# Performance work log

Measured on AMD Instinct MI355X. Metric: run time of the kernel, lower is better.

Reference implementation:

```python
import jax, jax.numpy as jnp
import numpy as np

DIM = 256
HEADS = 8
DIM_HEAD = 64
INNER = HEADS * DIM_HEAD  # 512
SCALE = DIM_HEAD ** -0.5
EPS = 1e-5


def _layernorm(x, w, b):
    mu = jnp.mean(x, axis=-1, keepdims=True)
    var = jnp.var(x, axis=-1, keepdims=True)
    return (x - mu) * jax.lax.rsqrt(var + EPS) * w + b


def setup_inputs() -> dict:
    key = jax.random.key(0)
    ks = jax.random.split(key, 20)
    B, N, M, H, W = 8, 4096, 256, 64, 64
    s = 0.02
    inp = {
        "feat": jax.random.normal(ks[0], (B, N, DIM), jnp.float32),
        "center": jax.random.normal(ks[1], (B, M, DIM), jnp.float32),
        "pos": jax.random.normal(ks[2], (B, DIM, H, W), jnp.float32),
        "center_pos": jax.random.normal(ks[3], (B, M, DIM), jnp.float32),
        # projection weights stored [in, out] so y = x @ W
        "Wq": jax.random.normal(ks[4], (DIM, INNER), jnp.float32) * s,
        "Wk": jax.random.normal(ks[5], (DIM, INNER), jnp.float32) * s,
        "Wv1": jax.random.normal(ks[6], (DIM, INNER), jnp.float32) * s,
        "Wv2": jax.random.normal(ks[7], (DIM, INNER), jnp.float32) * s,
        "Wo1": jax.random.normal(ks[8], (INNER, DIM), jnp.float32) * s,
        "Wo2": jax.random.normal(ks[9], (INNER, DIM), jnp.float32) * s,
        "ln1_w": jnp.ones((DIM,), jnp.float32),
        "ln1_b": jnp.zeros((DIM,), jnp.float32),
        "ln2_w": jnp.ones((DIM,), jnp.float32),
        "ln2_b": jnp.zeros((DIM,), jnp.float32),
        "ffn1_W1": jax.random.normal(ks[10], (DIM, DIM), jnp.float32) * s,
        "ffn1_W2": jax.random.normal(ks[11], (DIM, DIM), jnp.float32) * s,
        "ffn1_b2": jnp.zeros((DIM,), jnp.float32),
        "ffn2_W1": jax.random.normal(ks[12], (DIM, DIM), jnp.float32) * s,
        "ffn2_W2": jax.random.normal(ks[13], (DIM, DIM), jnp.float32) * s,
        "ffn2_b2": jnp.zeros((DIM,), jnp.float32),
    }
    return inp


def reference(feat, center, pos, center_pos, Wq, Wk, Wv1, Wv2, Wo1, Wo2,
              ln1_w, ln1_b, ln2_w, ln2_b, ffn1_W1, ffn1_W2, ffn1_b2,
              ffn2_W1, ffn2_W2, ffn2_b2):
    B = feat.shape[0]
    # pos: [B, C, H, W] -> [B, N, C]
    pos_f = pos.reshape(B, DIM, -1).transpose(0, 2, 1)
    q = (feat + pos_f) @ Wq            # [B, N, INNER]
    k = (center + center_pos) @ Wk     # [B, M, INNER]
    v1 = feat @ Wv1                    # [B, N, INNER]
    v2 = center @ Wv2                  # [B, M, INNER]

    def split(x):  # [B, T, h*d] -> [B, h, T, d]
        return x.reshape(B, x.shape[1], HEADS, DIM_HEAD).transpose(0, 2, 1, 3)

    q, k, v1, v2 = split(q), split(k), split(v1), split(v2)
    attn = jnp.einsum("bhnd,bhmd->bhnm", q, k) * SCALE  # [B, h, N, M]
    attn1 = jax.nn.softmax(attn, axis=-2)  # over N (queries)
    attn2 = jax.nn.softmax(attn, axis=-1)  # over M (keys)
    out_feat = jnp.einsum("bhnm,bhmd->bhnd", attn2, v2)    # [B, h, N, d]
    out_center = jnp.einsum("bhnm,bhnd->bhmd", attn1, v1)  # [B, h, M, d]

    def merge(x):  # [B, h, T, d] -> [B, T, h*d]
        return x.transpose(0, 2, 1, 3).reshape(B, x.shape[2], INNER)

    out_feat = merge(out_feat) @ Wo1 + feat
    out_center = merge(out_center) @ Wo2 + center
    out_feat = _layernorm(out_feat, ln1_w, ln1_b)
    out_center = _layernorm(out_center, ln2_w, ln2_b)
    out_feat = jax.nn.relu(out_feat @ ffn1_W1) @ ffn1_W2 + ffn1_b2 + out_feat
    out_center = jax.nn.relu(out_center @ ffn2_W1) @ ffn2_W2 + ffn2_b2 + out_center
    return out_feat, out_center
```

## Files before the change

### kernel.cpp

```cpp
#include <hip/hip_runtime.h>

typedef __bf16 bf16;
typedef __bf16 bf16x4 __attribute__((ext_vector_type(4)));
typedef __bf16 bf16x8 __attribute__((ext_vector_type(8)));
typedef float f32x4 __attribute__((ext_vector_type(4)));

#define MFMA16(a, b, c) __builtin_amdgcn_mfma_f32_16x16x32_bf16(a, b, c, 0, 0, 0)

#define CEXP 0.18033688011112042f

struct WTArgs {
  const float* src[10];
  bf16* dst[10];
  int K[10];
  int N[10];
};

__global__ __launch_bounds__(256) void wtrans_kernel(WTArgs args) {
  const int z = blockIdx.z;
  const int K = args.K[z], N = args.N[z];
  const int k0 = blockIdx.x * 64, n0 = blockIdx.y * 64;
  if (k0 >= K || n0 >= N) return;
  __shared__ float t[64][65];
  const int tx = threadIdx.x & 63, ty = threadIdx.x >> 6;
  const float* __restrict__ src = args.src[z];
  bf16* __restrict__ dst = args.dst[z];
#pragma unroll
  for (int i = 0; i < 16; ++i)
    t[ty + i * 4][tx] = src[(size_t)(k0 + ty + i * 4) * N + n0 + tx];
  __syncthreads();
#pragma unroll
  for (int i = 0; i < 16; ++i)
    dst[(size_t)(n0 + ty + i * 4) * K + k0 + tx] = (bf16)t[tx][ty + i * 4];
}

__global__ __launch_bounds__(256) void prep_xq_kernel(
    const float* __restrict__ feat, const float* __restrict__ pos,
    bf16* __restrict__ xq) {
  const int n0 = blockIdx.x * 64;
  const int c0 = blockIdx.y * 64;
  const int b = blockIdx.z;
  __shared__ float t[64][65];
  const int tx = threadIdx.x & 63, ty = threadIdx.x >> 6;
#pragma unroll
  for (int i = 0; i < 16; ++i) {
    int c = ty + i * 4;
    t[c][tx] = pos[((size_t)b * 256 + c0 + c) * 4096 + n0 + tx];
  }
  __syncthreads();
#pragma unroll
  for (int i = 0; i < 16; ++i) {
    int n = ty + i * 4;
    size_t off = ((size_t)b * 4096 + n0 + n) * 256 + c0 + tx;
    xq[off] = (bf16)(feat[off] + t[tx][n]);
  }
}

__device__ inline void stage16(const bf16* g, bf16* l) {
  __builtin_amdgcn_global_load_lds(
      (const __attribute__((address_space(1))) void*)g,
      (__attribute__((address_space(3))) void*)l, 16, 0, 0);
}

__device__ inline f32x4 rload(const float* p) { return *(const f32x4*)p; }
__device__ inline f32x4 rload(const bf16* p) {
  bf16x4 t = *(const bf16x4*)p;
  return (f32x4){(float)t[0], (float)t[1], (float)t[2], (float)t[3]};
}
__device__ inline void cstore(float* p, f32x4 v) { *(f32x4*)p = v; }
__device__ inline void cstore(bf16* p, f32x4 v) {
  bf16x4 o;
  o[0] = (bf16)v[0]; o[1] = (bf16)v[1]; o[2] = (bf16)v[2]; o[3] = (bf16)v[3];
  *(bf16x4*)p = o;
}

struct GArg {
  const void* A[2];
  const void* A2[2];
  const bf16* BT[2];
  void* C[2];
  const void* resid[2];
  const float* bias[2];
  int M[2];
};

template <int EPI, typename TO, typename TR, typename TA, bool FUSE2>
__global__ __launch_bounds__(256) void gemm_kernel(GArg g, int N, int K) {
  const int z = blockIdx.z;
  const int m0 = blockIdx.x * 128;
  if (m0 >= g.M[z]) return;
  constexpr bool F32A = sizeof(TA) == 4;
  const TA* A = (const TA*)g.A[z];
  const TA* A2 = (const TA*)g.A2[z];
  const bf16* BT = g.BT[z];
  TO* C = (TO*)g.C[z];
  const TR* resid = (const TR*)g.resid[z];
  const float* bias = g.bias[z];

  const int n0 = blockIdx.y * 128;
  const int tid = threadIdx.x;
  const int lane = tid & 63;
  const int w = tid >> 6;
  const int wr = (w >> 1) * 64, wc = (w & 1) * 64;
  const int l15 = lane & 15, quad = lane >> 4;

  __shared__ __align__(16) bf16 Al[2][128 * 32];
  __shared__ __align__(16) bf16 Bl[2][128 * 32];

  f32x4 acc[4][4];
#pragma unroll
  for (int i = 0; i < 4; ++i)
#pragma unroll
    for (int j = 0; j < 4; ++j) acc[i][j] = (f32x4){0.f, 0.f, 0.f, 0.f};

  const int sw = (((l15 >> 1) & 3) ^ quad) * 8;

  f32x4 ar[2][2], ar2[2][2];

  auto stageB = [&](int buf, int k0) {
#pragma unroll
    for (int c = 0; c < 2; ++c) {
      int idx = tid + c * 256;
      int row = idx >> 2;
      int gs = ((idx & 3) ^ ((row >> 1) & 3)) * 8;
      stage16(BT + (size_t)(n0 + row) * K + k0 + gs, Bl[buf] + idx * 8);
    }
  };
  auto stageA_dma = [&](int buf, int k0) {
    if constexpr (!F32A) {
#pragma unroll
      for (int c = 0; c < 2; ++c) {
        int idx = tid + c * 256;
        int row = idx >> 2;
        int gs = ((idx & 3) ^ ((row >> 1) & 3)) * 8;
        stage16((const bf16*)A + (size_t)(m0 + row) * K + k0 + gs,
                Al[buf] + idx * 8);
      }
    }
  };
  auto loadA = [&](int k0) {
    if constexpr (F32A) {
      const float* Af = (const float*)(const void*)A;
      const float* A2f = (const float*)(const void*)A2;
#pragma unroll
      for (int c = 0; c < 2; ++c) {
        int idx = tid + c * 256;
        int row = idx >> 2;
        int gs = ((idx & 3) ^ ((row >> 1) & 3)) * 8;
        const float* p = Af + (size_t)(m0 + row) * K + k0 + gs;
        ar[c][0] = *(const f32x4*)p;
        ar[c][1] = *((const f32x4*)p + 1);
        if constexpr (FUSE2) {
          const float* p2 = A2f + (size_t)(m0 + row) * K + k0 + gs;
          ar2[c][0] = *(const f32x4*)p2;
          ar2[c][1] = *((const f32x4*)p2 + 1);
        }
      }
    }
  };
  auto writeA = [&](int buf) {
    if constexpr (F32A) {
#pragma unroll
      for (int c = 0; c < 2; ++c) {
        int idx = tid + c * 256;
        f32x4 u = ar[c][0], v = ar[c][1];
        if constexpr (FUSE2) {
          u += ar2[c][0];
          v += ar2[c][1];
        }
        bf16x8 o;
#pragma unroll
        for (int e = 0; e < 4; ++e) {
          o[e] = (bf16)u[e];
          o[4 + e] = (bf16)v[e];
        }
        *(bf16x8*)(Al[buf] + idx * 8) = o;
      }
    }
  };

  if constexpr (F32A) {
    loadA(0);
    writeA(0);
  } else {
    stageA_dma(0, 0);
  }
  stageB(0, 0);

  int cur = 0;
  const int nt = K >> 5;
  for (int t = 0; t < nt; ++t) {
    __syncthreads();
    if (t + 1 < nt) {
      stageB(cur ^ 1, (t + 1) * 32);
      if constexpr (F32A)
        loadA((t + 1) * 32);
      else
        stageA_dma(cur ^ 1, (t + 1) * 32);
    }
    bf16x8 fa[4], fb[4];
#pragma unroll
    for (int i = 0; i < 4; ++i) {
      fa[i] = *(const bf16x8*)(Al[cur] + (wr + i * 16 + l15) * 32 + sw);
      fb[i] = *(const bf16x8*)(Bl[cur] + (wc + i * 16 + l15) * 32 + sw);
    }
#pragma unroll
    for (int i = 0; i < 4; ++i)
#pragma unroll
      for (int j = 0; j < 4; ++j)
        acc[i][j] = MFMA16(fb[j], fa[i], acc[i][j]);
    if constexpr (F32A) {
      if (t + 1 < nt) writeA(cur ^ 1);
    }
    cur ^= 1;
  }

#pragma unroll
  for (int i = 0; i < 4; ++i) {
#pragma unroll
    for (int j = 0; j < 4; ++j) {
      int row = m0 + wr + i * 16 + l15;
      int col = n0 + wc + j * 16 + quad * 4;
      size_t off = (size_t)row * N + col;
      f32x4 v = acc[i][j];
      if constexpr (EPI == 1) {
#pragma unroll
        for (int e = 0; e < 4; ++e) v[e] = fmaxf(v[e], 0.f);
      }
      if constexpr (EPI == 2) v += rload(resid + off);
      if constexpr (EPI == 3)
        v += rload(resid + off) + *(const f32x4*)(bias + col);
      cstore(C + off, v);
    }
  }
}

__global__ __launch_bounds__(256, 1) void attf_kernel(
    const bf16* q, const bf16* __restrict__ kk, const bf16* __restrict__ v1,
    const bf16* __restrict__ v2, bf16* af, float* __restrict__ acc_p,
    float* __restrict__ colsum_p) {
  const int nb = blockIdx.x;
  const int h = blockIdx.y;
  const int b = blockIdx.z;
  const int tid = threadIdx.x;
  const int lane = tid & 63;
  const int w = tid >> 6;
  const int l15 = lane & 15, quad = lane >> 4;

  __shared__ __align__(16) bf16 klds[256 * 72];
  __shared__ __align__(16) bf16 v2T[64 * 264];
  __shared__ __align__(16) bf16 v1T[2][64 * 72];
  __shared__ __align__(16) bf16 PT[256 * 72];

#pragma unroll
  for (int c = 0; c < 8; ++c) {
    int idx = tid + c * 256;
    int m = idx >> 3;
    int dc = (idx & 7) * 8;
    *(bf16x8*)(klds + m * 72 + dc) =
        *(const bf16x8*)(kk + ((size_t)(b * 256 + m)) * 512 + h * 64 + dc);
  }
#pragma unroll
  for (int c = 0; c < 8; ++c) {
    int idx = tid + c * 256;
    int m = idx >> 3;
    int dc = (idx & 7) * 8;
    bf16x8 t =
        *(const bf16x8*)(v2 + ((size_t)(b * 256 + m)) * 512 + h * 64 + dc);
    int p = (m & ~31) |
            (((((m >> 2) & 3) << 3) + (m & 3)) + (((m >> 4) & 1) << 2));
#pragma unroll
    for (int j = 0; j < 8; ++j) v2T[(dc + j) * 264 + p] = t[j];
  }
  {
    const int nl = tid >> 3;
    const int dc = (tid & 7) * 8;
    const bf16* v1b =
        v1 + ((size_t)(b * 4096 + nb * 1024)) * 512 + h * 64 + dc;
    bf16x8 t0 = *(const bf16x8*)(v1b + (size_t)nl * 512);
    bf16x8 t1 = *(const bf16x8*)(v1b + (size_t)(nl + 32) * 512);
#pragma unroll
    for (int j = 0; j < 8; ++j) {
      v1T[0][(dc + j) * 72 + nl] = t0[j];
      v1T[0][(dc + j) * 72 + nl + 32] = t1[j];
    }
  }
  bf16x8 qa0, qa1;
  {
    int nrow = b * 4096 + nb * 1024 + w * 16 + l15;
    const bf16* qp = q + (size_t)nrow * 512 + h * 64 + quad * 8;
    qa0 = *(const bf16x8*)(qp);
    qa1 = *(const bf16x8*)(qp + 32);
  }

  f32x4 oc2[16];
#pragma unroll
  for (int i = 0; i < 16; ++i) oc2[i] = (f32x4){0.f, 0.f, 0.f, 0.f};
  f32x4 csa[4];
#pragma unroll
  for (int i = 0; i < 4; ++i) csa[i] = (f32x4){0.f, 0.f, 0.f, 0.f};
  bf16x8 ones8;
#pragma unroll
  for (int j = 0; j < 8; ++j) ones8[j] = (bf16)1.0f;

  __syncthreads();

  for (int ch = 0; ch < 16; ++ch) {
    bf16x8 v1a, v1b;
    const int nl = tid >> 3;
    const int dc = (tid & 7) * 8;
    if (ch < 15) {
      const bf16* v1p =
          v1 + ((size_t)(b * 4096 + nb * 1024 + (ch + 1) * 64)) * 512 +
          h * 64 + dc;
      v1a = *(const bf16x8*)(v1p + (size_t)nl * 512);
      v1b = *(const bf16x8*)(v1p + (size_t)(nl + 32) * 512);
    }

    bf16x8 pa[8];
    float rs = 0.f;
#pragma unroll
    for (int mt = 0; mt < 16; ++mt) {
      const bf16* kp = klds + (mt * 16 + l15) * 72 + quad * 8;
      bf16x8 ka0 = *(const bf16x8*)(kp);
      bf16x8 ka1 = *(const bf16x8*)(kp + 32);
      f32x4 s = (f32x4){0.f, 0.f, 0.f, 0.f};
      s = MFMA16(ka0, qa0, s);
      s = MFMA16(ka1, qa1, s);
      float e0 = exp2f(s[0] * CEXP);
      float e1 = exp2f(s[1] * CEXP);
      float e2 = exp2f(s[2] * CEXP);
      float e3 = exp2f(s[3] * CEXP);
      rs += (e0 + e1) + (e2 + e3);
      bf16 b0 = (bf16)e0, b1 = (bf16)e1, b2 = (bf16)e2, b3 = (bf16)e3;
      int mrow = mt * 16 + quad * 4;
      PT[(mrow + 0) * 72 + w * 16 + l15] = b0;
      PT[(mrow + 1) * 72 + w * 16 + l15] = b1;
      PT[(mrow + 2) * 72 + w * 16 + l15] = b2;
      PT[(mrow + 3) * 72 + w * 16 + l15] = b3;
      pa[mt >> 1][(mt & 1) * 4 + 0] = b0;
      pa[mt >> 1][(mt & 1) * 4 + 1] = b1;
      pa[mt >> 1][(mt & 1) * 4 + 2] = b2;
      pa[mt >> 1][(mt & 1) * 4 + 3] = b3;
    }

    f32x4 o1[4];
#pragma unroll
    for (int i = 0; i < 4; ++i) o1[i] = (f32x4){0.f, 0.f, 0.f, 0.f};
#pragma unroll
    for (int ks = 0; ks < 8; ++ks) {
#pragma unroll
      for (int dt = 0; dt < 4; ++dt) {
        bf16x8 vb = *(const bf16x8*)(v2T + (dt * 16 + l15) * 264 + ks * 32 +
                                     quad * 8);
        o1[dt] = MFMA16(vb, pa[ks], o1[dt]);
      }
    }
    {
      float rsf = rs + __shfl_xor(rs, 16, 64);
      rsf += __shfl_xor(rsf, 32, 64);
      float inv = 1.f / rsf;
      int n = nb * 1024 + ch * 64 + w * 16 + l15;
      bf16* ap = af + ((size_t)(b * 4096 + n)) * 512 + h * 64 + quad * 4;
#pragma unroll
      for (int dt = 0; dt < 4; ++dt) {
        bf16x4 ov;
        ov[0] = (bf16)(o1[dt][0] * inv);
        ov[1] = (bf16)(o1[dt][1] * inv);
        ov[2] = (bf16)(o1[dt][2] * inv);
        ov[3] = (bf16)(o1[dt][3] * inv);
        *(bf16x4*)(ap + dt * 16) = ov;
      }
    }

    if (ch < 15) {
      bf16* dst = v1T[(ch + 1) & 1];
#pragma unroll
      for (int j = 0; j < 8; ++j) {
        dst[(dc + j) * 72 + nl] = v1a[j];
        dst[(dc + j) * 72 + nl + 32] = v1b[j];
      }
    }
    __syncthreads();

    bf16x8 qn0 = qa0, qn1 = qa1;
    if (ch < 15) {
      int nrow = b * 4096 + nb * 1024 + (ch + 1) * 64 + w * 16 + l15;
      const bf16* qp = q + (size_t)nrow * 512 + h * 64 + quad * 8;
      qn0 = *(const bf16x8*)(qp);
      qn1 = *(const bf16x8*)(qp + 32);
    }

    const bf16* vc = v1T[ch & 1];
#pragma unroll
    for (int ks = 0; ks < 2; ++ks) {
      bf16x8 vbv[4];
#pragma unroll
      for (int dt = 0; dt < 4; ++dt)
        vbv[dt] = *(const bf16x8*)(vc + (dt * 16 + l15) * 72 + ks * 32 +
                                   quad * 8);
#pragma unroll
      for (int mq = 0; mq < 4; ++mq) {
        bf16x8 pa2 = *(const bf16x8*)(PT + (mq * 64 + w * 16 + l15) * 72 +
                                      ks * 32 + quad * 8);
#pragma unroll
        for (int dt = 0; dt < 4; ++dt)
          oc2[mq * 4 + dt] = MFMA16(vbv[dt], pa2, oc2[mq * 4 + dt]);
        csa[mq] = MFMA16(pa2, ones8, csa[mq]);
      }
    }
    __syncthreads();
    qa0 = qn0;
    qa1 = qn1;
  }

  const size_t slab = (size_t)(nb * 64 + b * 8 + h);
  if (l15 == 0) {
#pragma unroll
    for (int mq = 0; mq < 4; ++mq)
#pragma unroll
      for (int r = 0; r < 4; ++r)
        colsum_p[slab * 256 + mq * 64 + w * 16 + quad * 4 + r] = csa[mq][r];
  }
  float* base = acc_p + slab * (256 * 64);
#pragma unroll
  for (int mq = 0; mq < 4; ++mq) {
    int m = mq * 64 + w * 16 + l15;
#pragma unroll
    for (int dt = 0; dt < 4; ++dt)
      *(f32x4*)(base + m * 64 + dt * 16 + quad * 4) = oc2[mq * 4 + dt];
  }
}

__global__ __launch_bounds__(256) void acm_kernel(
    const float* __restrict__ acc_p, const float* __restrict__ colsum_p,
    bf16* __restrict__ acm) {
  int idx = blockIdx.x * 256 + threadIdx.x;
  int d = idx & 63;
  int h = (idx >> 6) & 7;
  int m = (idx >> 9) & 255;
  int b = idx >> 17;
  float cv = 0.f, v = 0.f;
#pragma unroll
  for (int p = 0; p < 4; ++p) {
    cv += colsum_p[((size_t)(p * 64 + b * 8 + h)) * 256 + m];
    v += acc_p[(((size_t)(p * 64 + b * 8 + h)) * 256 + m) * 64 + d];
  }
  acm[idx] = (bf16)(v / cv);
}

__global__ __launch_bounds__(256) void ln_kernel(
    const bf16* __restrict__ x0, const bf16* __restrict__ x1,
    const float* __restrict__ w0, const float* __restrict__ b0,
    const float* __restrict__ w1, const float* __restrict__ b1,
    bf16* __restrict__ y0, bf16* __restrict__ y1, int rows0, int rows1) {
  int wave = threadIdx.x >> 6;
  int lane = threadIdx.x & 63;
  int row = blockIdx.x * 4 + wave;
  const bf16* x;
  const float *wv, *bv;
  bf16* y;
  if (row < rows0) {
    x = x0; wv = w0; bv = b0; y = y0;
  } else {
    row -= rows0;
    if (row >= rows1) return;
    x = x1; wv = w1; bv = b1; y = y1;
  }
  const bf16* xr = x + (size_t)row * 256;
  bf16x4 v = *(const bf16x4*)(xr + lane * 4);
  float f0 = v[0], f1 = v[1], f2 = v[2], f3 = v[3];
  float s = f0 + f1 + f2 + f3;
  float ss = f0 * f0 + f1 * f1 + f2 * f2 + f3 * f3;
#pragma unroll
  for (int m = 1; m < 64; m <<= 1) {
    s += __shfl_xor(s, m, 64);
    ss += __shfl_xor(ss, m, 64);
  }
  float mean = s * (1.f / 256.f);
  float var = ss * (1.f / 256.f) - mean * mean;
  float rstd = rsqrtf(var + 1e-5f);
  f32x4 wq = *(const f32x4*)(wv + lane * 4);
  f32x4 bq = *(const f32x4*)(bv + lane * 4);
  bf16x4 o;
  o[0] = (bf16)((f0 - mean) * rstd * wq[0] + bq[0]);
  o[1] = (bf16)((f1 - mean) * rstd * wq[1] + bq[1]);
  o[2] = (bf16)((f2 - mean) * rstd * wq[2] + bq[2]);
  o[3] = (bf16)((f3 - mean) * rstd * wq[3] + bq[3]);
  *(bf16x4*)(y + (size_t)row * 256 + lane * 4) = o;
}

extern "C" void kernel_launch(void* const* d_in, const int* in_sizes, int n_in,
                              void* d_out, int out_size, void* d_ws,
                              size_t ws_size, hipStream_t stream) {
  const float* feat = (const float*)d_in[0];
  const float* center = (const float*)d_in[1];
  const float* pos = (const float*)d_in[2];
  const float* cpos = (const float*)d_in[3];
  const float* Wq = (const float*)d_in[4];
  const float* Wk = (const float*)d_in[5];
  const float* Wv1 = (const float*)d_in[6];
  const float* Wv2 = (const float*)d_in[7];
  const float* Wo1 = (const float*)d_in[8];
  const float* Wo2 = (const float*)d_in[9];
  const float* ln1w = (const float*)d_in[10];
  const float* ln1b = (const float*)d_in[11];
  const float* ln2w = (const float*)d_in[12];
  const float* ln2b = (const float*)d_in[13];
  const float* f1W1 = (const float*)d_in[14];
  const float* f1W2 = (const float*)d_in[15];
  const float* f1b2 = (const float*)d_in[16];
  const float* f2W1 = (const float*)d_in[17];
  const float* f2W2 = (const float*)d_in[18];
  const float* f2b2 = (const float*)d_in[19];

  char* ws = (char*)d_ws;
  const size_t MB = 1024 * 1024;
  bf16* q_ = (bf16*)(ws + 0);
  bf16* af_ = q_;
  bf16* v1_ = (bf16*)(ws + 32 * MB);
  bf16* xq_ = (bf16*)(ws + 64 * MB);
  float* accp_ = (float*)(ws + 64 * MB);
  bf16* rf_ = xq_;
  bf16* k_ = (bf16*)(ws + 80 * MB);
  bf16* rc_ = (bf16*)(ws + 82 * MB);
  bf16* v2_ = (bf16*)(ws + 83 * MB);
  bf16* acm_ = v2_;
  float* colsum_ = (float*)(ws + 89 * MB);
  bf16* wt_ = (bf16*)(ws + 89 * MB + 262144);
  bf16* yf_ = q_;
  bf16* tf_ = (bf16*)(ws + 16 * MB);
  bf16* yc_ = (bf16*)(ws + 92 * MB);
  bf16* tc_ = (bf16*)(ws + 93 * MB);

  bf16* WqT = wt_;
  bf16* WkT = WqT + 131072;
  bf16* Wv1T = WkT + 131072;
  bf16* Wv2T = Wv1T + 131072;
  bf16* Wo1T = Wv2T + 131072;
  bf16* Wo2T = Wo1T + 131072;
  bf16* f1W1T = Wo2T + 131072;
  bf16* f1W2T = f1W1T + 65536;
  bf16* f2W1T = f1W2T + 65536;
  bf16* f2W2T = f2W1T + 65536;

  float* out_feat = (float*)d_out;
  float* out_center = out_feat + (size_t)8 * 4096 * 256;

  WTArgs wa;
  const float* srcs[10] = {Wq, Wk, Wv1, Wv2, Wo1, Wo2, f1W1, f1W2, f2W1, f2W2};
  bf16* dsts[10] = {WqT, WkT, Wv1T, Wv2T, Wo1T, Wo2T, f1W1T, f1W2T, f2W1T, f2W2T};
  int Ks[10] = {256, 256, 256, 256, 512, 512, 256, 256, 256, 256};
  int Ns[10] = {512, 512, 512, 512, 256, 256, 256, 256, 256, 256};
  for (int i = 0; i < 10; ++i) {
    wa.src[i] = srcs[i];
    wa.dst[i] = dsts[i];
    wa.K[i] = Ks[i];
    wa.N[i] = Ns[i];
  }

  wtrans_kernel<<<dim3(8, 8, 10), 256, 0, stream>>>(wa);
  prep_xq_kernel<<<dim3(64, 4, 8), 256, 0, stream>>>(feat, pos, xq_);

  {
    GArg a{};
    a.A[0] = xq_; a.BT[0] = WqT; a.C[0] = q_; a.M[0] = 32768;
    gemm_kernel<0, bf16, bf16, bf16, false>
        <<<dim3(256, 4, 1), 256, 0, stream>>>(a, 512, 256);
  }
  {
    GArg a{};
    a.A[0] = center; a.A2[0] = cpos; a.BT[0] = WkT; a.C[0] = k_;
    a.M[0] = 2048;
    gemm_kernel<0, bf16, bf16, float, true>
        <<<dim3(16, 4, 1), 256, 0, stream>>>(a, 512, 256);
  }
  {
    GArg a{};
    a.A[0] = feat; a.A[1] = center;
    a.BT[0] = Wv1T; a.BT[1] = Wv2T;
    a.C[0] = v1_; a.C[1] = v2_;
    a.M[0] = 32768; a.M[1] = 2048;
    gemm_kernel<0, bf16, bf16, float, false>
        <<<dim3(256, 4, 2), 256, 0, stream>>>(a, 512, 256);
  }

  attf_kernel<<<dim3(4, 8, 8), 256, 0, stream>>>(q_, k_, v1_, v2_, af_, accp_,
                                                 colsum_);
  acm_kernel<<<dim3(4096), 256, 0, stream>>>(accp_, colsum_, acm_);

  {
    GArg a{};
    a.A[0] = af_; a.A[1] = acm_;
    a.BT[0] = Wo1T; a.BT[1] = Wo2T;
    a.C[0] = rf_; a.C[1] = rc_;
    a.resid[0] = feat; a.resid[1] = center;
    a.M[0] = 32768; a.M[1] = 2048;
    gemm_kernel<2, bf16, float, bf16, false>
        <<<dim3(256, 2, 2), 256, 0, stream>>>(a, 256, 512);
  }
  ln_kernel<<<dim3(8704), 256, 0, stream>>>(rf_, rc_, ln1w, ln1b, ln2w, ln2b,
                                            yf_, yc_, 32768, 2048);
  {
    GArg a{};
    a.A[0] = yf_; a.A[1] = yc_;
    a.BT[0] = f1W1T; a.BT[1] = f2W1T;
    a.C[0] = tf_; a.C[1] = tc_;
    a.M[0] = 32768; a.M[1] = 2048;
    gemm_kernel<1, bf16, bf16, bf16, false>
        <<<dim3(256, 2, 2), 256, 0, stream>>>(a, 256, 256);
  }
  {
    GArg a{};
    a.A[0] = tf_; a.A[1] = tc_;
    a.BT[0] = f1W2T; a.BT[1] = f2W2T;
    a.C[0] = out_feat; a.C[1] = out_center;
    a.resid[0] = yf_; a.resid[1] = yc_;
    a.bias[0] = f1b2; a.bias[1] = f2b2;
    a.M[0] = 32768; a.M[1] = 2048;
    gemm_kernel<3, float, bf16, bf16, false>
        <<<dim3(256, 2, 2), 256, 0, stream>>>(a, 256, 256);
  }
}
```

Before: 354.7 us.

## Triple-buffer GEMM K-loop with explicit vmcnt waits and merge K projection launch

```diff
diff --git a/kernel.cpp b/kernel.cpp
--- a/kernel.cpp
+++ b/kernel.cpp
@@ -62,6 +62,16 @@
       (__attribute__((address_space(3))) void*)l, 16, 0, 0);
 }
 
+__device__ inline void wait_vm4() {
+  asm volatile("s_waitcnt vmcnt(4) lgkmcnt(0)" ::: "memory");
+}
+__device__ inline void wait_vm2() {
+  asm volatile("s_waitcnt vmcnt(2) lgkmcnt(0)" ::: "memory");
+}
+__device__ inline void wait_vm0() {
+  asm volatile("s_waitcnt vmcnt(0) lgkmcnt(0)" ::: "memory");
+}
+
 __device__ inline f32x4 rload(const float* p) { return *(const f32x4*)p; }
 __device__ inline f32x4 rload(const bf16* p) {
   bf16x4 t = *(const bf16x4*)p;
@@ -75,23 +85,23 @@
 }
 
 struct GArg {
-  const void* A[2];
-  const void* A2[2];
-  const bf16* BT[2];
-  void* C[2];
-  const void* resid[2];
-  const float* bias[2];
-  int M[2];
+  const void* A[3];
+  const void* A2[3];
+  const bf16* BT[3];
+  void* C[3];
+  const void* resid[3];
+  const float* bias[3];
+  int M[3];
 };
 
-template <int EPI, typename TO, typename TR, typename TA, bool FUSE2>
+template <int EPI, typename TO, typename TR, typename TA>
 __global__ __launch_bounds__(256) void gemm_kernel(GArg g, int N, int K) {
   const int z = blockIdx.z;
   const int m0 = blockIdx.x * 128;
   if (m0 >= g.M[z]) return;
   constexpr bool F32A = sizeof(TA) == 4;
   const TA* A = (const TA*)g.A[z];
-  const TA* A2 = (const TA*)g.A2[z];
+  const float* A2f = (const float*)g.A2[z];
   const bf16* BT = g.BT[z];
   TO* C = (TO*)g.C[z];
   const TR* resid = (const TR*)g.resid[z];
@@ -104,8 +114,8 @@
   const int wr = (w >> 1) * 64, wc = (w & 1) * 64;
   const int l15 = lane & 15, quad = lane >> 4;
 
-  __shared__ __align__(16) bf16 Al[2][128 * 32];
-  __shared__ __align__(16) bf16 Bl[2][128 * 32];
+  __shared__ __align__(16) bf16 Al[3][128 * 32];
+  __shared__ __align__(16) bf16 Bl[3][128 * 32];
 
   f32x4 acc[4][4];
 #pragma unroll
@@ -141,7 +151,6 @@
   auto loadA = [&](int k0) {
     if constexpr (F32A) {
       const float* Af = (const float*)(const void*)A;
-      const float* A2f = (const float*)(const void*)A2;
 #pragma unroll
       for (int c = 0; c < 2; ++c) {
         int idx = tid + c * 256;
@@ -150,7 +159,7 @@
         const float* p = Af + (size_t)(m0 + row) * K + k0 + gs;
         ar[c][0] = *(const f32x4*)p;
         ar[c][1] = *((const f32x4*)p + 1);
-        if constexpr (FUSE2) {
+        if (A2f) {
           const float* p2 = A2f + (size_t)(m0 + row) * K + k0 + gs;
           ar2[c][0] = *(const f32x4*)p2;
           ar2[c][1] = *((const f32x4*)p2 + 1);
@@ -164,7 +173,7 @@
       for (int c = 0; c < 2; ++c) {
         int idx = tid + c * 256;
         f32x4 u = ar[c][0], v = ar[c][1];
-        if constexpr (FUSE2) {
+        if (A2f) {
           u += ar2[c][0];
           v += ar2[c][1];
         }
@@ -182,27 +191,45 @@
   if constexpr (F32A) {
     loadA(0);
     writeA(0);
+    loadA(32);
+    writeA(1);
+    stageB(0, 0);
+    stageB(1, 32);
   } else {
     stageA_dma(0, 0);
-  }
-  stageB(0, 0);
-
-  int cur = 0;
+    stageB(0, 0);
+    stageA_dma(1, 32);
+    stageB(1, 32);
+  }
+
   const int nt = K >> 5;
   for (int t = 0; t < nt; ++t) {
-    __syncthreads();
     if (t + 1 < nt) {
-      stageB(cur ^ 1, (t + 1) * 32);
       if constexpr (F32A)
-        loadA((t + 1) * 32);
+        wait_vm2();
       else
-        stageA_dma(cur ^ 1, (t + 1) * 32);
-    }
+        wait_vm4();
+    } else {
+      wait_vm0();
+    }
+    __builtin_amdgcn_s_barrier();
+    __builtin_amdgcn_sched_barrier(0);
+    if (t + 2 < nt) {
+      int nb = (t + 2) % 3;
+      if constexpr (F32A) {
+        loadA((t + 2) * 32);
+        stageB(nb, (t + 2) * 32);
+      } else {
+        stageA_dma(nb, (t + 2) * 32);
+        stageB(nb, (t + 2) * 32);
+      }
+    }
+    const int cb = t % 3;
     bf16x8 fa[4], fb[4];
 #pragma unroll
     for (int i = 0; i < 4; ++i) {
-      fa[i] = *(const bf16x8*)(Al[cur] + (wr + i * 16 + l15) * 32 + sw);
-      fb[i] = *(const bf16x8*)(Bl[cur] + (wc + i * 16 + l15) * 32 + sw);
+      fa[i] = *(const bf16x8*)(Al[cb] + (wr + i * 16 + l15) * 32 + sw);
+      fb[i] = *(const bf16x8*)(Bl[cb] + (wc + i * 16 + l15) * 32 + sw);
     }
 #pragma unroll
     for (int i = 0; i < 4; ++i)
@@ -210,9 +237,8 @@
       for (int j = 0; j < 4; ++j)
         acc[i][j] = MFMA16(fb[j], fa[i], acc[i][j]);
     if constexpr (F32A) {
-      if (t + 1 < nt) writeA(cur ^ 1);
-    }
-    cur ^= 1;
+      if (t + 2 < nt) writeA((t + 2) % 3);
+    }
   }
 
 #pragma unroll
@@ -565,24 +591,18 @@
   {
     GArg a{};
     a.A[0] = xq_; a.BT[0] = WqT; a.C[0] = q_; a.M[0] = 32768;
-    gemm_kernel<0, bf16, bf16, bf16, false>
+    gemm_kernel<0, bf16, bf16, bf16>
         <<<dim3(256, 4, 1), 256, 0, stream>>>(a, 512, 256);
   }
   {
     GArg a{};
-    a.A[0] = center; a.A2[0] = cpos; a.BT[0] = WkT; a.C[0] = k_;
-    a.M[0] = 2048;
-    gemm_kernel<0, bf16, bf16, float, true>
-        <<<dim3(16, 4, 1), 256, 0, stream>>>(a, 512, 256);
-  }
-  {
-    GArg a{};
-    a.A[0] = feat; a.A[1] = center;
-    a.BT[0] = Wv1T; a.BT[1] = Wv2T;
-    a.C[0] = v1_; a.C[1] = v2_;
-    a.M[0] = 32768; a.M[1] = 2048;
-    gemm_kernel<0, bf16, bf16, float, false>
-        <<<dim3(256, 4, 2), 256, 0, stream>>>(a, 512, 256);
+    a.A[0] = feat; a.A[1] = center; a.A[2] = center;
+    a.A2[2] = cpos;
+    a.BT[0] = Wv1T; a.BT[1] = Wv2T; a.BT[2] = WkT;
+    a.C[0] = v1_; a.C[1] = v2_; a.C[2] = k_;
+    a.M[0] = 32768; a.M[1] = 2048; a.M[2] = 2048;
+    gemm_kernel<0, bf16, bf16, float>
+        <<<dim3(256, 4, 3), 256, 0, stream>>>(a, 512, 256);
   }
 
   attf_kernel<<<dim3(4, 8, 8), 256, 0, stream>>>(q_, k_, v1_, v2_, af_, accp_,
@@ -596,7 +616,7 @@
     a.C[0] = rf_; a.C[1] = rc_;
     a.resid[0] = feat; a.resid[1] = center;
     a.M[0] = 32768; a.M[1] = 2048;
-    gemm_kernel<2, bf16, float, bf16, false>
+    gemm_kernel<2, bf16, float, bf16>
         <<<dim3(256, 2, 2), 256, 0, stream>>>(a, 256, 512);
   }
   ln_kernel<<<dim3(8704), 256, 0, stream>>>(rf_, rc_, ln1w, ln1b, ln2w, ln2b,
@@ -607,7 +627,7 @@
     a.BT[0] = f1W1T; a.BT[1] = f2W1T;
     a.C[0] = tf_; a.C[1] = tc_;
     a.M[0] = 32768; a.M[1] = 2048;
-    gemm_kernel<1, bf16, bf16, bf16, false>
+    gemm_kernel<1, bf16, bf16, bf16>
         <<<dim3(256, 2, 2), 256, 0, stream>>>(a, 256, 256);
   }
   {
@@ -618,7 +638,7 @@
     a.resid[0] = yf_; a.resid[1] = yc_;
     a.bias[0] = f1b2; a.bias[1] = f2b2;
     a.M[0] = 32768; a.M[1] = 2048;
-    gemm_kernel<3, float, bf16, bf16, false>
+    gemm_kernel<3, float, bf16, bf16>
         <<<dim3(256, 2, 2), 256, 0, stream>>>(a, 256, 256);
   }
 }
```

After: 351.9 us. Within noise of the previous version (-0.8%).
